# Performance work log

Measured on AMD Instinct MI355X. Metric: run time of the kernel, lower is better.

## Reference

```python
import jax, jax.numpy as jnp
import numpy as np

WINDOW = 128
BACKWARD = 1
FORWARD = 0

def look_around(x, pad_value):
    # x: [b, windows, window_size, ...]; pad window axis and gather shifted windows
    w = x.shape[1]
    pads = [(0, 0), (BACKWARD, FORWARD)] + [(0, 0)] * (x.ndim - 2)
    p = jnp.pad(x, pads, constant_values=pad_value)
    return jnp.concatenate([p[:, i:i + w] for i in range(BACKWARD + FORWARD + 1)], axis=2)

def setup_inputs() -> dict:
    key = jax.random.key(0)
    ks = jax.random.split(key, 5)
    shp = (2, 16, 4096, 64)
    names = ['q', 'k', 'q_rot', 'k_rot', 'v']
    inp = {n: jax.random.normal(ks[i], shp, dtype=jnp.float32) for i, n in enumerate(names)}
    inp['states'] = 0
    inp['inferring_states'] = 0
    return inp

def reference(q, k, q_rot, k_rot, v, states, inferring_states):
    shape = q.shape
    merge = lambda t: t.reshape(-1, t.shape[-2], t.shape[-1])
    q, k, q_rot, k_rot, v = map(merge, (q, k, q_rot, k_rot, v))
    b, t, e = q.shape
    windows = t // WINDOW
    ticker = jnp.arange(t, dtype=q.dtype)[None, :]
    b_t = ticker.reshape(1, windows, WINDOW)
    bucket = lambda x: x.reshape(b, windows, WINDOW, e)
    bq, bk, bq_rot, bk_rot, bv = map(bucket, (q, k, q_rot, k_rot, v))
    bk = look_around(bk, 0.0)
    bk_rot = look_around(bk_rot, 0.0)
    bv = look_around(bv, 0.0)
    bq_t = b_t
    bq_k = look_around(b_t, -1.0)
    scale = e ** (-0.5)
    dots = jnp.einsum('bwie,bwje->bwij', bq, bk) * scale
    dots_rot = jnp.einsum('bwie,bwje->bwij', bq_rot, bk_rot) * scale
    mask_value = -jnp.finfo(dots.dtype).max
    causal_mask = bq_t[:, :, :, None] < bq_k[:, :, None, :]
    pad_mask = bq_k[:, :, None, :] == -1
    mask = causal_mask | pad_mask
    dots = jnp.where(mask, mask_value, dots)
    dots_rot = jnp.where(mask, mask_value, dots_rot)
    attn = jax.nn.softmax(dots + dots_rot, axis=-1)
    out = jnp.einsum('bwij,bwje->bwie', attn, bv)
    return out.reshape(shape)
```

## Files before the change

### kernel.cpp

```cpp
#include <hip/hip_runtime.h>
#include <stdint.h>

#define T 4096
#define E 64
#define NWIN 32
#define NBH 32
#define KK_LD 136
#define VT_LD 264
#define PB_STRIDE (16*264)
#define KK_BYTES 69632
#define SMEM_BYTES 103424

typedef __attribute__((ext_vector_type(8))) short short8;
typedef __attribute__((ext_vector_type(4))) short short4v;
typedef __attribute__((ext_vector_type(4))) float f32x4;

__device__ __forceinline__ short f2bf(float x) {
  unsigned u = __float_as_uint(x);
  u += 0x7fffu + ((u >> 16) & 1u);
  return (short)(u >> 16);
}

__global__ __launch_bounds__(512, 2)
void la_kernel(const float* __restrict__ qg, const float* __restrict__ kg,
               const float* __restrict__ qrg, const float* __restrict__ krg,
               const float* __restrict__ vg, float* __restrict__ outg) {
  extern __shared__ char smem[];
  short* KK = (short*)smem;
  short* Pb = (short*)smem;
  short* Vt = (short*)(smem + KK_BYTES);

  const int w   = blockIdx.x;
  const int bh  = blockIdx.y;
  const int tid = threadIdx.x;
  const int wid  = tid >> 6;
  const int lane = tid & 63;
  const int li = lane & 15;
  const int lg = lane >> 4;

  const size_t base = (size_t)bh * T * E;
  const int krow0 = w * 128 - 128;

  const int qrow = w * 128 + wid * 16 + li;
  const float* qp  = qg  + base + (size_t)qrow * E;
  const float* qrp = qrg + base + (size_t)qrow * E;
  short8 aF[4];
#pragma unroll
  for (int kt = 0; kt < 4; ++kt) {
    const float* sp = (kt < 2 ? qp : qrp) + (kt & 1) * 32 + lg * 8;
    float4 f0 = *(const float4*)sp;
    float4 f1 = *(const float4*)(sp + 4);
    short8 a;
    a[0]=f2bf(f0.x*0.125f); a[1]=f2bf(f0.y*0.125f); a[2]=f2bf(f0.z*0.125f); a[3]=f2bf(f0.w*0.125f);
    a[4]=f2bf(f1.x*0.125f); a[5]=f2bf(f1.y*0.125f); a[6]=f2bf(f1.z*0.125f); a[7]=f2bf(f1.w*0.125f);
    aF[kt] = a;
  }

#pragma unroll
  for (int m = 0; m < 2; ++m) {
    const float* src = m ? krg : kg;
#pragma unroll
    for (int it = 0; it < 8; ++it) {
      int idx = it * 512 + tid;
      int row = idx >> 4, c4 = idx & 15;
      int grow = krow0 + row;
      float4 f = make_float4(0.f, 0.f, 0.f, 0.f);
      if (grow >= 0) f = *(const float4*)(src + base + (size_t)grow * E + c4 * 4);
      short4v h = { f2bf(f.x), f2bf(f.y), f2bf(f.z), f2bf(f.w) };
      *(short4v*)(KK + row * KK_LD + m * 64 + c4 * 4) = h;
    }
  }
#pragma unroll
  for (int it = 0; it < 8; ++it) {
    int idx = it * 512 + tid;
    int row = idx >> 4, c4 = idx & 15;
    int grow = krow0 + row;
    float4 f = make_float4(0.f, 0.f, 0.f, 0.f);
    if (grow >= 0) f = *(const float4*)(vg + base + (size_t)grow * E + c4 * 4);
    Vt[(c4*4+0)*VT_LD + row] = f2bf(f.x);
    Vt[(c4*4+1)*VT_LD + row] = f2bf(f.y);
    Vt[(c4*4+2)*VT_LD + row] = f2bf(f.z);
    Vt[(c4*4+3)*VT_LD + row] = f2bf(f.w);
  }
  __syncthreads();

  f32x4 S[16];
#pragma unroll
  for (int ct = 0; ct < 16; ++ct) {
    f32x4 acc = {0.f, 0.f, 0.f, 0.f};
    const short* kb = KK + (ct * 16 + li) * KK_LD + lg * 8;
#pragma unroll
    for (int kt = 0; kt < 4; ++kt) {
      short8 b = *(const short8*)(kb + kt * 32);
      acc = __builtin_amdgcn_mfma_f32_16x16x32_bf16(aF[kt], b, acc, 0, 0, 0);
    }
    S[ct] = acc;
  }

  const int rowb = wid * 16 + lg * 4;
  float linv[4];
#pragma unroll
  for (int r = 0; r < 4; ++r) {
    const int qi = rowb + r;
    float mx = -1e30f;
#pragma unroll
    for (int ct = 0; ct < 16; ++ct) {
      int jj = ct * 16 + li;
      bool valid = (jj <= qi + 128) && (w > 0 || jj >= 128);
      float sv = valid ? S[ct][r] : -1e30f;
      S[ct][r] = sv;
      mx = fmaxf(mx, sv);
    }
    mx = fmaxf(mx, __shfl_xor(mx, 1));
    mx = fmaxf(mx, __shfl_xor(mx, 2));
    mx = fmaxf(mx, __shfl_xor(mx, 4));
    mx = fmaxf(mx, __shfl_xor(mx, 8));
    float sm = 0.f;
#pragma unroll
    for (int ct = 0; ct < 16; ++ct) {
      float e = __expf(S[ct][r] - mx);
      S[ct][r] = e;
      sm += e;
    }
    sm += __shfl_xor(sm, 1);
    sm += __shfl_xor(sm, 2);
    sm += __shfl_xor(sm, 4);
    sm += __shfl_xor(sm, 8);
    linv[r] = 1.f / sm;
  }
  __syncthreads();

  short* pw = Pb + wid * PB_STRIDE;
#pragma unroll
  for (int ct = 0; ct < 16; ++ct) {
#pragma unroll
    for (int r = 0; r < 4; ++r) {
      pw[(lg * 4 + r) * 264 + ct * 16 + li] = f2bf(S[ct][r]);
    }
  }
  __syncthreads();

  short8 aP[8];
  const short* pr = Pb + wid * PB_STRIDE + li * 264 + lg * 8;
#pragma unroll
  for (int kt = 0; kt < 8; ++kt) aP[kt] = *(const short8*)(pr + kt * 32);
  f32x4 O[4] = {{0,0,0,0},{0,0,0,0},{0,0,0,0},{0,0,0,0}};
#pragma unroll
  for (int kt = 0; kt < 8; ++kt) {
#pragma unroll
    for (int nt = 0; nt < 4; ++nt) {
      short8 b = *(const short8*)(Vt + (nt * 16 + li) * VT_LD + kt * 32 + lg * 8);
      O[nt] = __builtin_amdgcn_mfma_f32_16x16x32_bf16(aP[kt], b, O[nt], 0, 0, 0);
    }
  }

  float* op = outg + base + (size_t)(w * 128 + rowb) * E;
#pragma unroll
  for (int r = 0; r < 4; ++r) {
#pragma unroll
    for (int nt = 0; nt < 4; ++nt) {
      op[(size_t)r * E + nt * 16 + li] = O[nt][r] * linv[r];
    }
  }
}

extern "C" void kernel_launch(void* const* d_in, const int* in_sizes, int n_in,
                              void* d_out, int out_size, void* d_ws, size_t ws_size,
                              hipStream_t stream) {
  const float* q  = (const float*)d_in[0];
  const float* k  = (const float*)d_in[1];
  const float* qr = (const float*)d_in[2];
  const float* kr = (const float*)d_in[3];
  const float* v  = (const float*)d_in[4];
  float* out = (float*)d_out;
  dim3 grid(NWIN, NBH);
  la_kernel<<<grid, dim3(512), SMEM_BYTES, stream>>>(q, k, qr, kr, v, out);
}
```

Measured before the change: 238.2 us.

## Stream V in two halves through shared memory to cut LDS footprint

The separate V-transpose buffer is no longer held alongside K. V is loaded and transposed into shared memory in two 128-row chunks after the softmax, and the P tile and the PV MFMA product are split to match, so K, V and P can reuse a smaller shared region. This lowers the LDS requirement to about 69.6KB and raises the launch bound to four blocks per CU to allow more occupancy. In exchange it adds extra barriers, moves V loading after the QK and softmax stage, and loads V with strided per-row scalar reads. With higher occupancy the register budget is also tighter, so spills are possible.

```diff
diff --git a/kernel.cpp b/kernel.cpp
--- a/kernel.cpp
+++ b/kernel.cpp
@@ -6,10 +6,10 @@
 #define NWIN 32
 #define NBH 32
 #define KK_LD 136
-#define VT_LD 264
-#define PB_STRIDE (16*264)
-#define KK_BYTES 69632
-#define SMEM_BYTES 103424
+#define VT_LD 136
+#define PB_STRIDE (16*136)
+#define VT_BYTES (64*136*2)
+#define SMEM_BYTES (256*136*2)
 
 typedef __attribute__((ext_vector_type(8))) short short8;
 typedef __attribute__((ext_vector_type(4))) short short4v;
@@ -21,14 +21,14 @@
   return (short)(u >> 16);
 }
 
-__global__ __launch_bounds__(512, 2)
+__global__ __launch_bounds__(512, 4)
 void la_kernel(const float* __restrict__ qg, const float* __restrict__ kg,
                const float* __restrict__ qrg, const float* __restrict__ krg,
                const float* __restrict__ vg, float* __restrict__ outg) {
   extern __shared__ char smem[];
   short* KK = (short*)smem;
-  short* Pb = (short*)smem;
-  short* Vt = (short*)(smem + KK_BYTES);
+  short* Vt = (short*)smem;
+  short* Pb = (short*)(smem + VT_BYTES);
 
   const int w   = blockIdx.x;
   const int bh  = blockIdx.y;
@@ -69,18 +69,6 @@
       short4v h = { f2bf(f.x), f2bf(f.y), f2bf(f.z), f2bf(f.w) };
       *(short4v*)(KK + row * KK_LD + m * 64 + c4 * 4) = h;
     }
-  }
-#pragma unroll
-  for (int it = 0; it < 8; ++it) {
-    int idx = it * 512 + tid;
-    int row = idx >> 4, c4 = idx & 15;
-    int grow = krow0 + row;
-    float4 f = make_float4(0.f, 0.f, 0.f, 0.f);
-    if (grow >= 0) f = *(const float4*)(vg + base + (size_t)grow * E + c4 * 4);
-    Vt[(c4*4+0)*VT_LD + row] = f2bf(f.x);
-    Vt[(c4*4+1)*VT_LD + row] = f2bf(f.y);
-    Vt[(c4*4+2)*VT_LD + row] = f2bf(f.z);
-    Vt[(c4*4+3)*VT_LD + row] = f2bf(f.w);
   }
   __syncthreads();
 
@@ -130,28 +118,48 @@
   }
   __syncthreads();
 
-  short* pw = Pb + wid * PB_STRIDE;
+  f32x4 O[4] = {{0,0,0,0},{0,0,0,0},{0,0,0,0},{0,0,0,0}};
+#pragma unroll 1
+  for (int c = 0; c < 2; ++c) {
+    const bool active = (w > 0) || (c == 1);
+    if (active) {
+      const int rb2 = wid * 16;
+      const float* vp = vg + base + (size_t)(krow0 + c * 128 + rb2) * E + lane;
 #pragma unroll
-  for (int ct = 0; ct < 16; ++ct) {
+      for (int rq = 0; rq < 4; ++rq) {
+        short4v h;
 #pragma unroll
-    for (int r = 0; r < 4; ++r) {
-      pw[(lg * 4 + r) * 264 + ct * 16 + li] = f2bf(S[ct][r]);
+        for (int j = 0; j < 4; ++j) {
+          h[j] = f2bf(vp[(size_t)(rq * 4 + j) * E]);
+        }
+        *(short4v*)(Vt + lane * VT_LD + rb2 + rq * 4) = h;
+      }
+      short* pw = Pb + wid * PB_STRIDE;
+#pragma unroll
+      for (int cc = 0; cc < 8; ++cc) {
+        const int ct = c * 8 + cc;
+#pragma unroll
+        for (int r = 0; r < 4; ++r) {
+          pw[(lg * 4 + r) * VT_LD + cc * 16 + li] = f2bf(S[ct][r]);
+        }
+      }
     }
-  }
-  __syncthreads();
-
-  short8 aP[8];
-  const short* pr = Pb + wid * PB_STRIDE + li * 264 + lg * 8;
+    __syncthreads();
+    if (active) {
+      short8 aP[4];
+      const short* pr = Pb + wid * PB_STRIDE + li * VT_LD + lg * 8;
 #pragma unroll
-  for (int kt = 0; kt < 8; ++kt) aP[kt] = *(const short8*)(pr + kt * 32);
-  f32x4 O[4] = {{0,0,0,0},{0,0,0,0},{0,0,0,0},{0,0,0,0}};
+      for (int kt = 0; kt < 4; ++kt) aP[kt] = *(const short8*)(pr + kt * 32);
 #pragma unroll
-  for (int kt = 0; kt < 8; ++kt) {
+      for (int kt = 0; kt < 4; ++kt) {
 #pragma unroll
-    for (int nt = 0; nt < 4; ++nt) {
-      short8 b = *(const short8*)(Vt + (nt * 16 + li) * VT_LD + kt * 32 + lg * 8);
-      O[nt] = __builtin_amdgcn_mfma_f32_16x16x32_bf16(aP[kt], b, O[nt], 0, 0, 0);
+        for (int nt = 0; nt < 4; ++nt) {
+          short8 b = *(const short8*)(Vt + (nt * 16 + li) * VT_LD + kt * 32 + lg * 8);
+          O[nt] = __builtin_amdgcn_mfma_f32_16x16x32_bf16(aP[kt], b, O[nt], 0, 0, 0);
+        }
+      }
     }
+    __syncthreads();
   }
 
   float* op = outg + base + (size_t)(w * 128 + rowb) * E;
```

After: 252.6 us. +6.1%, slower.
